# Optimization experiments

Measured on AMD Instinct MI355X. Metric: run time of the kernel, lower is better.

The kernel has to match this reference:

```python
import jax, jax.numpy as jnp
import numpy as np
import math

B, T, C, H = 2, 2048, 1024, 16
HD = C // H

def setup_inputs() -> dict:
    key = jax.random.key(0)
    ks = jax.random.split(key, 5)
    s_in = 1.0 / math.sqrt(C)
    x = jax.random.normal(ks[0], (B, T, C), dtype=jnp.float32)
    W_attn = jax.random.normal(ks[1], (C, 3 * C), dtype=jnp.float32) * s_in
    b_attn = jnp.zeros((3 * C,), dtype=jnp.float32)
    W_proj = jax.random.normal(ks[2], (C, C), dtype=jnp.float32) * s_in
    b_proj = jnp.zeros((C,), dtype=jnp.float32)
    return {"x": x, "W_attn": W_attn, "b_attn": b_attn, "W_proj": W_proj, "b_proj": b_proj}

def reference(x, W_attn, b_attn, W_proj, b_proj):
    Bx, Tx, Cx = x.shape
    c = x @ W_attn + b_attn  # [B,T,3C]
    q, k, v = jnp.split(c, 3, axis=2)
    # [B,T,H,hd] -> [B,H,T,hd]
    q = q.reshape(Bx, Tx, H, HD).transpose(0, 2, 1, 3)
    k = k.reshape(Bx, Tx, H, HD).transpose(0, 2, 1, 3)
    v = v.reshape(Bx, Tx, H, HD).transpose(0, 2, 1, 3)
    # NOTE: module scales by 1/sqrt(C), not 1/sqrt(head_dim)
    attn = jnp.einsum('bhqd,bhkd->bhqk', q, k) * (1.0 / math.sqrt(Cx))
    causal = jnp.tril(jnp.ones((Tx, Tx), dtype=bool))
    attn = jnp.where(causal[None, None], attn, -jnp.inf)
    attn = jax.nn.softmax(attn, axis=-1)
    y = jnp.einsum('bhqk,bhkd->bhqd', attn, v)
    y = y.transpose(0, 2, 1, 3).reshape(Bx, Tx, Cx)
    return y @ W_proj + b_proj
```

## Files before the change

kernel.cpp:

```cpp
#include <hip/hip_runtime.h>
#include <math.h>

#define Bv 2
#define Tv 2048
#define Cv 1024
#define Hv 16
#define HDv 64
#define Mv (Bv * Tv)
#define SZv (Bv * Hv * Tv * HDv)

typedef short bf16x8 __attribute__((ext_vector_type(8)));
typedef float f32x4 __attribute__((ext_vector_type(4)));

static __device__ __forceinline__ unsigned short f2bf(float f) {
    unsigned u = __float_as_uint(f);
    u += 0x7fffu + ((u >> 16) & 1u);
    return (unsigned short)(u >> 16);
}

static __device__ __forceinline__ unsigned f2bf2(float a, float b) {
    unsigned r;
    asm("v_cvt_pk_bf16_f32 %0, %1, %2" : "=v"(r) : "v"(a), "v"(b));
    return r;
}

#define AS1 __attribute__((address_space(1)))
#define AS3 __attribute__((address_space(3)))
#define GLD16(gp, lp) __builtin_amdgcn_global_load_lds( \
    (AS1 const void*)(const void*)(gp), (AS3 void*)(void*)(lp), 16, 0, 0)

#define WAITVM(n) asm volatile("s_waitcnt vmcnt(" #n ")" ::: "memory")
#define BARRIER   asm volatile("s_barrier" ::: "memory")

__global__ __launch_bounds__(256) void prep_kernel(
    const float* __restrict__ x, const float* __restrict__ Wa,
    const float* __restrict__ Wp,
    unsigned short* __restrict__ xB, unsigned short* __restrict__ WaT,
    unsigned short* __restrict__ WpT)
{
    __shared__ float tile[32][33];
    const int bid = blockIdx.x;
    const int tid = threadIdx.x;

    if (bid < 4096) {
        int i = bid * 256 + tid;
        float4 f = ((const float4*)x)[i];
        ushort4 u;
        u.x = f2bf(f.x); u.y = f2bf(f.y); u.z = f2bf(f.z); u.w = f2bf(f.w);
        ((ushort4*)xB)[i] = u;
        return;
    }
    const float* src; unsigned short* dst; int Ncols, bi;
    if (bid < 7168) { bi = bid - 4096; Ncols = 3072; src = Wa; dst = WaT; }
    else            { bi = bid - 7168; Ncols = 1024; src = Wp; dst = WpT; }
    const int nct = Ncols / 32;
    const int c0 = (bi % nct) * 32, r0 = (bi / nct) * 32;
    const int tx = tid & 31, ty = tid >> 5;
    #pragma unroll
    for (int i = 0; i < 4; ++i)
        tile[ty + i * 8][tx] = src[(size_t)(r0 + ty + i * 8) * Ncols + c0 + tx];
    __syncthreads();
    #pragma unroll
    for (int i = 0; i < 4; ++i)
        dst[(size_t)(c0 + ty + i * 8) * Cv + r0 + tx] = f2bf(tile[tx][ty + i * 8]);
}

template<int AG>
__device__ __forceinline__ void mm_mainloop_1024(
    const unsigned short* __restrict__ A, const unsigned short* __restrict__ Bt,
    unsigned short* lds, int rowBase, int colBase, f32x4 acc[][4])
{
    const int tid  = threadIdx.x;
    const int lane = tid & 63;
    const int w    = tid >> 6;
    const int quad = lane >> 4, l15 = lane & 15;
    const int wm = (w >> 1) * (32 * AG), wn = (w & 1) * 64;
    const int K = 1024;
    constexpr int ASZ = 2048 * AG;
    constexpr int BUF = ASZ + 4096;
    constexpr int MI  = 2 * AG;

    size_t offA[AG]; unsigned short* ldsA[AG];
    size_t offB[2];  unsigned short* ldsB[2];
    #pragma unroll
    for (int i = 0; i < AG; ++i) {
        int g = w * (64 * AG) + i * 64 + lane;
        int r = g >> 2, kc = (g & 3) ^ ((r >> 1) & 3);
        offA[i] = (size_t)(rowBase + r) * K + kc * 8;
        ldsA[i] = lds + (w * AG + i) * 512;
    }
    #pragma unroll
    for (int i = 0; i < 2; ++i) {
        int g = w * 128 + i * 64 + lane;
        int r = g >> 2, kc = (g & 3) ^ ((r >> 1) & 3);
        offB[i] = (size_t)(colBase + r) * K + kc * 8;
        ldsB[i] = lds + ASZ + (w * 2 + i) * 512;
    }

    const int sw = quad ^ ((l15 >> 1) & 3);
    int aoff[MI], boff[4];
    #pragma unroll
    for (int i = 0; i < MI; ++i) aoff[i] = ((wm + i * 16 + l15) * 4 + sw) * 8;
    #pragma unroll
    for (int i = 0; i < 4; ++i)  boff[i] = ASZ + ((wn + i * 16 + l15) * 4 + sw) * 8;

    #pragma unroll
    for (int t = 0; t < 2; ++t) {
        #pragma unroll
        for (int i = 0; i < AG; ++i) GLD16(A + offA[i] + t * 32, ldsA[i] + t * BUF);
        #pragma unroll
        for (int i = 0; i < 2; ++i)  GLD16(Bt + offB[i] + t * 32, ldsB[i] + t * BUF);
    }

    int cur = 0;
    for (int i = 0; i < 32; ++i) {
        if (i < 31) {
            if constexpr (AG == 2) { WAITVM(4); } else { WAITVM(3); }
        } else { WAITVM(0); }
        BARRIER;
        if (i < 30) {
            int nb = cur + 2 * BUF; if (nb >= 3 * BUF) nb -= 3 * BUF;
            const int k2 = (i + 2) * 32;
            #pragma unroll
            for (int ai = 0; ai < AG; ++ai) GLD16(A + offA[ai] + k2, ldsA[ai] + nb);
            #pragma unroll
            for (int bi = 0; bi < 2; ++bi)  GLD16(Bt + offB[bi] + k2, ldsB[bi] + nb);
        }

        bf16x8 a[MI], b[4];
        #pragma unroll
        for (int j = 0; j < MI; ++j) a[j] = *(const bf16x8*)(lds + cur + aoff[j]);
        #pragma unroll
        for (int j = 0; j < 4; ++j)  b[j] = *(const bf16x8*)(lds + cur + boff[j]);

        #pragma unroll
        for (int mi = 0; mi < MI; ++mi)
            #pragma unroll
            for (int ni = 0; ni < 4; ++ni)
                acc[mi][ni] = __builtin_amdgcn_mfma_f32_16x16x32_bf16(
                    a[mi], b[ni], acc[mi][ni], 0, 0, 0);

        cur += BUF; if (cur == 3 * BUF) cur = 0;
    }
}

__global__ __launch_bounds__(256) void qkv_mm_kernel(
    const unsigned short* __restrict__ xB, const unsigned short* __restrict__ WaT,
    const float* __restrict__ bias,
    unsigned short* __restrict__ qB, unsigned short* __restrict__ kB,
    unsigned short* __restrict__ vT)
{
    __shared__ __align__(16) unsigned short lds[24576];
    const int rowBase = blockIdx.y * 128;
    const int colBase = blockIdx.x * 128;

    f32x4 acc[4][4];
    #pragma unroll
    for (int i = 0; i < 4; ++i)
        #pragma unroll
        for (int j = 0; j < 4; ++j) acc[i][j] = (f32x4){0.f, 0.f, 0.f, 0.f};

    mm_mainloop_1024<2>(xB, WaT, lds, rowBase, colBase, acc);
    __syncthreads();

    const int tid = threadIdx.x, lane = tid & 63, w = tid >> 6;
    const int quad = lane >> 4, l15 = lane & 15;
    const int wm = (w >> 1) * 64, wn = (w & 1) * 64;
    const int s = colBase / Cv;
    const int tloc = rowBase & (Tv - 1);
    const int bh0 = (rowBase / Tv) * Hv + (colBase % Cv) / HDv;

    if (s < 2) {
        const float qs = (s == 0) ? 0.04508422f : 1.0f;
        #pragma unroll
        for (int mi = 0; mi < 4; ++mi)
            #pragma unroll
            for (int ni = 0; ni < 4; ++ni) {
                float bv = bias[colBase + wn + ni * 16 + l15];
                #pragma unroll
                for (int r = 0; r < 4; ++r) {
                    int m = wm + mi * 16 + quad * 4 + r;
                    int n = wn + ni * 16 + l15;
                    lds[m * 136 + n] = f2bf((acc[mi][ni][r] + bv) * qs);
                }
            }
        __syncthreads();
        unsigned short* dst = (s == 0) ? qB : kB;
        #pragma unroll
        for (int it = 0; it < 8; ++it) {
            int cc = tid + it * 256;
            int m = cc >> 4, j = cc & 15;
            uint4 v = *(const uint4*)(lds + m * 136 + j * 8);
            int hh = j >> 3, d0 = (j & 7) * 8;
            *(uint4*)(dst + ((size_t)(bh0 + hh) * Tv + tloc + m) * HDv + d0) = v;
        }
    } else {
        #pragma unroll
        for (int mi = 0; mi < 4; ++mi)
            #pragma unroll
            for (int ni = 0; ni < 4; ++ni) {
                float bv = bias[colBase + wn + ni * 16 + l15];
                #pragma unroll
                for (int r = 0; r < 4; ++r) {
                    int m = wm + mi * 16 + quad * 4 + r;
                    int mk = m & 31;
                    int mp = (m & ~31) | (mk & 3) | (((mk >> 4) & 1) << 2)
                           | (((mk >> 2) & 3) << 3);
                    int n = wn + ni * 16 + l15;
                    lds[n * 136 + mp] = f2bf(acc[mi][ni][r] + bv);
                }
            }
        __syncthreads();
        #pragma unroll
        for (int it = 0; it < 8; ++it) {
            int cc = tid + it * 256;
            int n = cc >> 4, j = cc & 15;
            uint4 v = *(const uint4*)(lds + n * 136 + j * 8);
            int hh = n >> 6, d = n & 63;
            *(uint4*)(vT + ((size_t)(bh0 + hh) * HDv + d) * Tv + tloc + j * 8) = v;
        }
    }
}

__global__ __launch_bounds__(256) void proj_mm_kernel(
    const unsigned short* __restrict__ y0B, const unsigned short* __restrict__ WpT,
    const float* __restrict__ bias, float* __restrict__ out)
{
    __shared__ __align__(16) unsigned short lds[18432];
    const int rowBase = blockIdx.y * 64;
    const int colBase = blockIdx.x * 128;

    f32x4 acc[2][4];
    #pragma unroll
    for (int i = 0; i < 2; ++i)
        #pragma unroll
        for (int j = 0; j < 4; ++j) acc[i][j] = (f32x4){0.f, 0.f, 0.f, 0.f};

    mm_mainloop_1024<1>(y0B, WpT, lds, rowBase, colBase, acc);

    const int tid = threadIdx.x, lane = tid & 63, w = tid >> 6;
    const int quad = lane >> 4, l15 = lane & 15;
    const int wm = (w >> 1) * 32, wn = (w & 1) * 64;

    #pragma unroll
    for (int mi = 0; mi < 2; ++mi)
        #pragma unroll
        for (int ni = 0; ni < 4; ++ni) {
            int n = colBase + wn + ni * 16 + l15;
            float bv = bias[n];
            #pragma unroll
            for (int r = 0; r < 4; ++r) {
                int m = rowBase + wm + mi * 16 + quad * 4 + r;
                out[(size_t)m * Cv + n] = acc[mi][ni][r] + bv;
            }
        }
}

__global__ __launch_bounds__(256, 3) void attn_kernel(
    const unsigned short* __restrict__ qB, const unsigned short* __restrict__ kB,
    const unsigned short* __restrict__ vT, unsigned short* __restrict__ y0B)
{
    __shared__ __align__(16) unsigned short kv[3 * 8192];

    const int tid  = threadIdx.x;
    const int lane = tid & 63;
    const int w    = tid >> 6;
    const int quad = lane >> 4;
    const int l15  = lane & 15;

    const int bid = blockIdx.x;
    const int idx = bid & 255;
    const int qt  = (bid & 256) ? (idx >> 5) : (15 - (idx >> 5));
    const int bh  = idx & 31;

    const int ktmax = 2 * qt + 1;
    const int ktw   = 2 * qt + (w >> 1);
    const int qbase = qt * 128 + w * 32;

    bf16x8 Qf[2][2];
    #pragma unroll
    for (int rg = 0; rg < 2; ++rg) {
        const unsigned short* qrow =
            qB + ((size_t)bh * Tv + qbase + rg * 16 + l15) * HDv;
        Qf[rg][0] = *(const bf16x8*)(qrow + quad * 8);
        Qf[rg][1] = *(const bf16x8*)(qrow + 32 + quad * 8);
    }
    WAITVM(0);

    f32x4 O[2][4];
    float l[2] = {0.f, 0.f};
    #pragma unroll
    for (int rg = 0; rg < 2; ++rg)
        #pragma unroll
        for (int n = 0; n < 4; ++n) O[rg][n] = (f32x4){0.f, 0.f, 0.f, 0.f};

    const unsigned short* Kbase = kB + (size_t)bh * Tv * HDv;
    const unsigned short* Vbase = vT + (size_t)bh * HDv * Tv;

    const unsigned short* gK[2]; unsigned short* dK[2];
    const unsigned short* gV[2]; unsigned short* dV[2];
    #pragma unroll
    for (int i = 0; i < 2; ++i) {
        int slot = tid + i * 256;
        int row = slot >> 3;
        int gk = (slot & 7) ^ (row & 7);
        gK[i] = Kbase + row * HDv + gk * 8;
        dK[i] = kv + (size_t)(i * 256 + w * 64) * 8;
        int d = slot >> 3;
        int gv = (slot & 7) ^ (d & 7);
        gV[i] = Vbase + (size_t)d * Tv + gv * 8;
        dV[i] = kv + 4096 + (size_t)(i * 256 + w * 64) * 8;
    }

    int koff[4][2], voff[4][2];
    #pragma unroll
    for (int ct = 0; ct < 4; ++ct)
        #pragma unroll
        for (int jj = 0; jj < 2; ++jj)
            koff[ct][jj] = ((ct * 16 + l15) * 8 + ((jj * 4 + quad) ^ (l15 & 7))) * 8;
    #pragma unroll
    for (int nt = 0; nt < 4; ++nt)
        #pragma unroll
        for (int hh = 0; hh < 2; ++hh)
            voff[nt][hh] = 4096 + ((nt * 16 + l15) * 8 + ((quad + 4 * hh) ^ (l15 & 7))) * 8;

#define STAGE(t, bufoff) do { \
    GLD16(gK[0] + (size_t)(t) * 64 * HDv, dK[0] + (bufoff)); \
    GLD16(gK[1] + (size_t)(t) * 64 * HDv, dK[1] + (bufoff)); \
    GLD16(gV[0] + (t) * 64, dV[0] + (bufoff)); \
    GLD16(gV[1] + (t) * 64, dV[1] + (bufoff)); \
} while (0)

    STAGE(0, 0);
    STAGE(1, 8192);

    int cur = 0;
    for (int kt = 0; kt <= ktmax; ++kt) {
        if (kt < ktmax) { WAITVM(4); } else { WAITVM(0); }
        BARRIER;
        if (kt + 2 <= ktmax) {
            int nb = cur + 16384; if (nb >= 24576) nb -= 24576;
            STAGE(kt + 2, nb);
        }

        if (kt <= ktw) {
            const unsigned short* kvc = kv + cur;
            #pragma unroll
            for (int hh = 0; hh < 2; ++hh) {
                bf16x8 Kb[2][2];
                #pragma unroll
                for (int c2 = 0; c2 < 2; ++c2) {
                    int ct = hh * 2 + c2;
                    Kb[c2][0] = *(const bf16x8*)(kvc + koff[ct][0]);
                    Kb[c2][1] = *(const bf16x8*)(kvc + koff[ct][1]);
                }
                bf16x8 Vb[4];
                #pragma unroll
                for (int nt = 0; nt < 4; ++nt)
                    Vb[nt] = *(const bf16x8*)(kvc + voff[nt][hh]);

                f32x4 S[2][2];
                #pragma unroll
                for (int rg = 0; rg < 2; ++rg)
                    #pragma unroll
                    for (int c2 = 0; c2 < 2; ++c2) {
                        S[rg][c2] = (f32x4){0.f, 0.f, 0.f, 0.f};
                        S[rg][c2] = __builtin_amdgcn_mfma_f32_16x16x32_bf16(
                            Kb[c2][0], Qf[rg][0], S[rg][c2], 0, 0, 0);
                        S[rg][c2] = __builtin_amdgcn_mfma_f32_16x16x32_bf16(
                            Kb[c2][1], Qf[rg][1], S[rg][c2], 0, 0, 0);
                    }

                if (kt == ktw) {
                    const int kb2 = (w >> 1) * 64 + hh * 32;
                    #pragma unroll
                    for (int rg = 0; rg < 2; ++rg) {
                        const int rrel = w * 32 + rg * 16 + l15;
                        #pragma unroll
                        for (int c2 = 0; c2 < 2; ++c2)
                            #pragma unroll
                            for (int r = 0; r < 4; ++r)
                                if (kb2 + c2 * 16 + quad * 4 + r > rrel)
                                    S[rg][c2][r] = -1e30f;
                    }
                }

                #pragma unroll
                for (int rg = 0; rg < 2; ++rg) {
                    float p0[4], p1[4];
                    #pragma unroll
                    for (int r = 0; r < 4; ++r) {
                        p0[r] = __builtin_amdgcn_exp2f(S[rg][0][r]);
                        p1[r] = __builtin_amdgcn_exp2f(S[rg][1][r]);
                    }
                    l[rg] += ((p0[0] + p0[1]) + (p0[2] + p0[3]))
                           + ((p1[0] + p1[1]) + (p1[2] + p1[3]));

                    union { unsigned u[4]; bf16x8 v; } pa;
                    pa.u[0] = f2bf2(p0[0], p0[1]);
                    pa.u[1] = f2bf2(p0[2], p0[3]);
                    pa.u[2] = f2bf2(p1[0], p1[1]);
                    pa.u[3] = f2bf2(p1[2], p1[3]);
                    #pragma unroll
                    for (int nt = 0; nt < 4; ++nt)
                        O[rg][nt] = __builtin_amdgcn_mfma_f32_16x16x32_bf16(
                            pa.v, Vb[nt], O[rg][nt], 0, 0, 0);
                }
            }
        }

        cur += 8192; if (cur == 24576) cur = 0;
    }
#undef STAGE

    #pragma unroll
    for (int rg = 0; rg < 2; ++rg) {
        l[rg] += __shfl_xor(l[rg], 16);
        l[rg] += __shfl_xor(l[rg], 32);
    }

    const int b = bh >> 4, h = bh & 15;
    #pragma unroll
    for (int rg = 0; rg < 2; ++rg)
        #pragma unroll
        for (int r = 0; r < 4; ++r) {
            float lr = __shfl(l[rg], quad * 4 + r);
            float inv = 1.f / lr;
            int q = qbase + rg * 16 + quad * 4 + r;
            unsigned short* dst = y0B + ((size_t)(b * Tv + q)) * Cv + h * HDv + l15;
            #pragma unroll
            for (int nt = 0; nt < 4; ++nt) dst[nt * 16] = f2bf(O[rg][nt][r] * inv);
        }
}

extern "C" void kernel_launch(void* const* d_in, const int* in_sizes, int n_in,
                              void* d_out, int out_size, void* d_ws, size_t ws_size,
                              hipStream_t stream) {
    const float* x      = (const float*)d_in[0];
    const float* W_attn = (const float*)d_in[1];
    const float* b_attn = (const float*)d_in[2];
    const float* W_proj = (const float*)d_in[3];
    const float* b_proj = (const float*)d_in[4];
    float* out = (float*)d_out;

    unsigned short* xB  = (unsigned short*)d_ws;
    unsigned short* WaT = xB  + (size_t)Mv * Cv;
    unsigned short* WpT = WaT + (size_t)3 * Cv * Cv;
    unsigned short* qB  = WpT + (size_t)Cv * Cv;
    unsigned short* kB  = qB + (size_t)SZv;
    unsigned short* vT  = kB + (size_t)SZv;
    unsigned short* y0B = vT + (size_t)SZv;

    dim3 blk(256);
    prep_kernel<<<dim3(8192), blk, 0, stream>>>(x, W_attn, W_proj, xB, WaT, WpT);
    qkv_mm_kernel<<<dim3(3 * Cv / 128, Mv / 128), blk, 0, stream>>>(xB, WaT, b_attn, qB, kB, vT);
    attn_kernel<<<dim3(32 * 16), blk, 0, stream>>>(qB, kB, vT, y0B);
    proj_mm_kernel<<<dim3(Cv / 128, Mv / 64), blk, 0, stream>>>(y0B, WpT, b_proj, out);
}
```

Measured before the change: 163.0 us.

## Software-pipeline attention PV MFMAs one key tile behind QK and softmax

Restructures the attention inner loop so the P·V MFMAs for the previous key tile are issued alongside the current tile's QK MFMAs and exp2 work. The previous tile's P fragments and V fragments are carried in registers, with an epilogue that drains the last tile. The goal is to overlap matrix-core work with the transcendental and conversion work instead of serialising them. Holding all four K fragments and the extra P/V registers raises register pressure, so launch bounds drop from 3 to 2 blocks per CU, which lowers occupancy.

```diff
diff --git a/kernel.cpp b/kernel.cpp
--- a/kernel.cpp
+++ b/kernel.cpp
@@ -256,7 +256,7 @@
         }
 }
 
-__global__ __launch_bounds__(256, 3) void attn_kernel(
+__global__ __launch_bounds__(256, 2) void attn_kernel(
     const unsigned short* __restrict__ qB, const unsigned short* __restrict__ kB,
     const unsigned short* __restrict__ vT, unsigned short* __restrict__ y0B)
 {
@@ -334,6 +334,9 @@
     STAGE(0, 0);
     STAGE(1, 8192);
 
+    bf16x8 Pprev[2][2];
+    bf16x8 Vprev[2][4];
+
     int cur = 0;
     for (int kt = 0; kt <= ktmax; ++kt) {
         if (kt < ktmax) { WAITVM(4); } else { WAITVM(0); }
@@ -345,33 +348,46 @@
 
         if (kt <= ktw) {
             const unsigned short* kvc = kv + cur;
-            #pragma unroll
-            for (int hh = 0; hh < 2; ++hh) {
-                bf16x8 Kb[2][2];
-                #pragma unroll
-                for (int c2 = 0; c2 < 2; ++c2) {
-                    int ct = hh * 2 + c2;
-                    Kb[c2][0] = *(const bf16x8*)(kvc + koff[ct][0]);
-                    Kb[c2][1] = *(const bf16x8*)(kvc + koff[ct][1]);
-                }
-                bf16x8 Vb[4];
-                #pragma unroll
-                for (int nt = 0; nt < 4; ++nt)
-                    Vb[nt] = *(const bf16x8*)(kvc + voff[nt][hh]);
-
-                f32x4 S[2][2];
+            bf16x8 Kb[4][2];
+            #pragma unroll
+            for (int ct = 0; ct < 4; ++ct) {
+                Kb[ct][0] = *(const bf16x8*)(kvc + koff[ct][0]);
+                Kb[ct][1] = *(const bf16x8*)(kvc + koff[ct][1]);
+            }
+            f32x4 S[2][2][2];
+            #pragma unroll
+            for (int hh = 0; hh < 2; ++hh)
                 #pragma unroll
                 for (int rg = 0; rg < 2; ++rg)
                     #pragma unroll
                     for (int c2 = 0; c2 < 2; ++c2) {
-                        S[rg][c2] = (f32x4){0.f, 0.f, 0.f, 0.f};
-                        S[rg][c2] = __builtin_amdgcn_mfma_f32_16x16x32_bf16(
-                            Kb[c2][0], Qf[rg][0], S[rg][c2], 0, 0, 0);
-                        S[rg][c2] = __builtin_amdgcn_mfma_f32_16x16x32_bf16(
-                            Kb[c2][1], Qf[rg][1], S[rg][c2], 0, 0, 0);
+                        S[hh][rg][c2] = (f32x4){0.f, 0.f, 0.f, 0.f};
+                        S[hh][rg][c2] = __builtin_amdgcn_mfma_f32_16x16x32_bf16(
+                            Kb[hh * 2 + c2][0], Qf[rg][0], S[hh][rg][c2], 0, 0, 0);
+                        S[hh][rg][c2] = __builtin_amdgcn_mfma_f32_16x16x32_bf16(
+                            Kb[hh * 2 + c2][1], Qf[rg][1], S[hh][rg][c2], 0, 0, 0);
                     }
 
-                if (kt == ktw) {
+            if (kt > 0) {
+                #pragma unroll
+                for (int hh = 0; hh < 2; ++hh)
+                    #pragma unroll
+                    for (int rg = 0; rg < 2; ++rg)
+                        #pragma unroll
+                        for (int nt = 0; nt < 4; ++nt)
+                            O[rg][nt] = __builtin_amdgcn_mfma_f32_16x16x32_bf16(
+                                Pprev[hh][rg], Vprev[hh][nt], O[rg][nt], 0, 0, 0);
+            }
+
+            #pragma unroll
+            for (int hh = 0; hh < 2; ++hh)
+                #pragma unroll
+                for (int nt = 0; nt < 4; ++nt)
+                    Vprev[hh][nt] = *(const bf16x8*)(kvc + voff[nt][hh]);
+
+            if (kt == ktw) {
+                #pragma unroll
+                for (int hh = 0; hh < 2; ++hh) {
                     const int kb2 = (w >> 1) * 64 + hh * 32;
                     #pragma unroll
                     for (int rg = 0; rg < 2; ++rg) {
@@ -381,37 +397,55 @@
                             #pragma unroll
                             for (int r = 0; r < 4; ++r)
                                 if (kb2 + c2 * 16 + quad * 4 + r > rrel)
-                                    S[rg][c2][r] = -1e30f;
+                                    S[hh][rg][c2][r] = -1e30f;
                     }
                 }
-
+            }
+
+            #pragma unroll
+            for (int hh = 0; hh < 2; ++hh)
                 #pragma unroll
                 for (int rg = 0; rg < 2; ++rg) {
                     float p0[4], p1[4];
                     #pragma unroll
                     for (int r = 0; r < 4; ++r) {
-                        p0[r] = __builtin_amdgcn_exp2f(S[rg][0][r]);
-                        p1[r] = __builtin_amdgcn_exp2f(S[rg][1][r]);
+                        p0[r] = __builtin_amdgcn_exp2f(S[hh][rg][0][r]);
+                        p1[r] = __builtin_amdgcn_exp2f(S[hh][rg][1][r]);
                     }
                     l[rg] += ((p0[0] + p0[1]) + (p0[2] + p0[3]))
                            + ((p1[0] + p1[1]) + (p1[2] + p1[3]));
-
                     union { unsigned u[4]; bf16x8 v; } pa;
                     pa.u[0] = f2bf2(p0[0], p0[1]);
                     pa.u[1] = f2bf2(p0[2], p0[3]);
                     pa.u[2] = f2bf2(p1[0], p1[1]);
                     pa.u[3] = f2bf2(p1[2], p1[3]);
+                    Pprev[hh][rg] = pa.v;
+                }
+        } else if (kt == ktw + 1) {
+            #pragma unroll
+            for (int hh = 0; hh < 2; ++hh)
+                #pragma unroll
+                for (int rg = 0; rg < 2; ++rg)
                     #pragma unroll
                     for (int nt = 0; nt < 4; ++nt)
                         O[rg][nt] = __builtin_amdgcn_mfma_f32_16x16x32_bf16(
-                            pa.v, Vb[nt], O[rg][nt], 0, 0, 0);
-                }
-            }
+                            Pprev[hh][rg], Vprev[hh][nt], O[rg][nt], 0, 0, 0);
         }
 
         cur += 8192; if (cur == 24576) cur = 0;
     }
 #undef STAGE
+
+    if (ktw == ktmax) {
+        #pragma unroll
+        for (int hh = 0; hh < 2; ++hh)
+            #pragma unroll
+            for (int rg = 0; rg < 2; ++rg)
+                #pragma unroll
+                for (int nt = 0; nt < 4; ++nt)
+                    O[rg][nt] = __builtin_amdgcn_mfma_f32_16x16x32_bf16(
+                        Pprev[hh][rg], Vprev[hh][nt], O[rg][nt], 0, 0, 0);
+    }
 
     #pragma unroll
     for (int rg = 0; rg < 2; ++rg) {
```

Result: no change. 163.4 us (+0.2%).
